# Kernel optimization log

Hardware: AMD Instinct MI355X
Metric: run time of the kernel (lower is better)

Reference implementation:

```python
import jax, jax.numpy as jnp
import numpy as np

MD = 4  # max displacement -> 9x9 = 81 window, matches the +8 pad and 81 output channels


def setup_inputs() -> dict:
    key = jax.random.key(0)
    k1, k2 = jax.random.split(key)
    first = jax.random.normal(k1, (8, 256, 96, 128), dtype=jnp.float32)
    second = jax.random.normal(k2, (8, 256, 96, 128), dtype=jnp.float32)
    return {"first": first, "second": second}


def reference(first, second):
    # first, second: [B, C, H, W]
    B, C, H, W = first.shape
    # pad second spatially by MD on each side (the rbot1 [B, H+8, W+8, C] buffer)
    pad = jnp.pad(second, ((0, 0), (0, 0), (MD, MD), (MD, MD)))
    outs = []
    # channel ordering matches CUDA kernel: top_channel = (dy+4)*9 + (dx+4)
    for dy in range(2 * MD + 1):
        for dx in range(2 * MD + 1):
            shifted = jax.lax.dynamic_slice(pad, (0, 0, dy, dx), (B, C, H, W))
            outs.append(jnp.einsum('bchw,bchw->bhw', first, shifted))
    # kernel divides the per-pixel dot product by the channel count
    return jnp.stack(outs, axis=1) / C  # [B, 81, H, W]
```

## Files before the change

### kernel.cpp

```cpp
#include <hip/hip_runtime.h>

namespace {
constexpr int Bn = 8, Cn = 256, Hn = 96, Wn = 128;
constexpr int HWn = Hn * Wn;
constexpr int CHWn = Cn * HWn;
constexpr int ND = 9;
constexpr int STRIDE = 140;
constexpr int TILESH = Hn / 4;
constexpr int NBLK = Bn * TILESH * ND;
constexpr int PERX = NBLK / 8;
}

__global__ __launch_bounds__(64) void corr_kernel(
    const float* __restrict__ first, const float* __restrict__ second,
    float* __restrict__ out)
{
  __shared__ __align__(16) float sbuf[2][4 * STRIDE];

  const int lane = threadIdx.x;
  const int bid = blockIdx.x;
  const int logical = (bid & 7) * PERX + (bid >> 3);
  const int dy = logical % ND;
  const int t = logical / ND;
  const int b = t / TILESH;
  const int h0 = (t % TILESH) * 4;

  const int hs = lane >> 4;
  const int w0 = (lane & 15) << 3;

  const int r0 = lane >> 5;
  const int cc = lane & 31;

  const int gr0 = h0 + dy - 4 + r0;
  const int gr1 = gr0 + 2;
  const float m0 = (gr0 >= 0 && gr0 < Hn) ? 1.0f : 0.0f;
  const float m1 = (gr1 >= 0 && gr1 < Hn) ? 1.0f : 0.0f;
  const int cg0 = min(max(gr0, 0), Hn - 1);
  const int cg1 = min(max(gr1, 0), Hn - 1);

  const float* src0 = second + b * CHWn + cg0 * Wn + 4 * cc;
  const float* src1 = second + b * CHWn + cg1 * Wn + 4 * cc;
  const float* fsrc = first + b * CHWn + (h0 + hs) * Wn + w0;

  const int dw0 = STRIDE * r0 + 4 + 4 * cc;
  const int dw1 = STRIDE * (r0 + 2) + 4 + 4 * cc;
  const int srw = STRIDE * hs + w0;

  if (lane < 16) {
    const int bsel = lane >> 3;
    const int row = (lane >> 1) & 3;
    const int side = lane & 1;
    *(float4*)&sbuf[bsel][STRIDE * row + (side ? 132 : 0)] =
        make_float4(0.f, 0.f, 0.f, 0.f);
  }

  float acc[ND][8];
#pragma unroll
  for (int dx = 0; dx < ND; ++dx)
#pragma unroll
    for (int p = 0; p < 8; ++p) acc[dx][p] = 0.f;

  float4 st0 = *(const float4*)src0;
  float4 st1 = *(const float4*)src1;
  float4 fa = *(const float4*)fsrc;
  float4 fb = *(const float4*)(fsrc + 4);
  src0 += HWn; src1 += HWn; fsrc += HWn;
  st0.x *= m0; st0.y *= m0; st0.z *= m0; st0.w *= m0;
  st1.x *= m1; st1.y *= m1; st1.z *= m1; st1.w *= m1;
  *(float4*)&sbuf[0][dw0] = st0;
  *(float4*)&sbuf[0][dw1] = st1;

#pragma unroll 2
  for (int c = 0; c < Cn; ++c) {
    const int cur = c & 1;
    float4 nst0, nst1, nfa, nfb;
    if (c < Cn - 1) {
      nst0 = *(const float4*)src0;
      nst1 = *(const float4*)src1;
      nfa = *(const float4*)fsrc;
      nfb = *(const float4*)(fsrc + 4);
      src0 += HWn; src1 += HWn; fsrc += HWn;
    } else {
      nst0 = nst1 = nfa = nfb = make_float4(0.f, 0.f, 0.f, 0.f);
    }

    const float* sb = &sbuf[cur][srw];
    float4 q0 = *(const float4*)(sb + 0);
    float4 q1 = *(const float4*)(sb + 4);
    float4 q2 = *(const float4*)(sb + 8);
    float4 q3 = *(const float4*)(sb + 12);
    const float s[16] = {q0.x, q0.y, q0.z, q0.w, q1.x, q1.y, q1.z, q1.w,
                         q2.x, q2.y, q2.z, q2.w, q3.x, q3.y, q3.z, q3.w};
    const float f[8] = {fa.x, fa.y, fa.z, fa.w, fb.x, fb.y, fb.z, fb.w};

#pragma unroll
    for (int dx = 0; dx < ND; ++dx)
#pragma unroll
      for (int p = 0; p < 8; ++p)
        acc[dx][p] = fmaf(f[p], s[p + dx], acc[dx][p]);

    if (c < Cn - 1) {
      nst0.x *= m0; nst0.y *= m0; nst0.z *= m0; nst0.w *= m0;
      nst1.x *= m1; nst1.y *= m1; nst1.z *= m1; nst1.w *= m1;
      const int nxt = cur ^ 1;
      *(float4*)&sbuf[nxt][dw0] = nst0;
      *(float4*)&sbuf[nxt][dw1] = nst1;
    }
    fa = nfa; fb = nfb;
  }

  const float sc = 1.0f / Cn;
  float* obase = out + ((b * 81 + dy * ND) * Hn + (h0 + hs)) * Wn + w0;
#pragma unroll
  for (int dx = 0; dx < ND; ++dx) {
    float4 o0 = make_float4(acc[dx][0] * sc, acc[dx][1] * sc,
                            acc[dx][2] * sc, acc[dx][3] * sc);
    float4 o1 = make_float4(acc[dx][4] * sc, acc[dx][5] * sc,
                            acc[dx][6] * sc, acc[dx][7] * sc);
    *(float4*)(obase + dx * HWn) = o0;
    *(float4*)(obase + dx * HWn + 4) = o1;
  }
}

extern "C" void kernel_launch(void* const* d_in, const int* in_sizes, int n_in,
                              void* d_out, int out_size, void* d_ws, size_t ws_size,
                              hipStream_t stream) {
  const float* first = (const float*)d_in[0];
  const float* second = (const float*)d_in[1];
  float* out = (float*)d_out;
  corr_kernel<<<dim3(NBLK), dim3(64), 0, stream>>>(first, second, out);
}
```

Before: 120.7 us.

## Replace LDS staging of shifted rows with DPP lane shifts and deeper prefetch

Each lane now loads its own 8 values of the padded second-image row and gets the 4 left and 4 right neighbours from adjacent lanes through DPP row_shr/row_shl moves. This removes the shared-memory double buffer along with its writes and reads, and out-of-range edge lanes are zero-filled by bound_ctrl. The channel loop now prefetches two channels ahead with explicit register staging, and launch bounds request 2 blocks per CU. In exchange there are more VALU moves per channel and higher register pressure from the larger prefetch.

```diff
diff --git a/kernel.cpp b/kernel.cpp
--- a/kernel.cpp
+++ b/kernel.cpp
@@ -5,18 +5,28 @@
 constexpr int HWn = Hn * Wn;
 constexpr int CHWn = Cn * HWn;
 constexpr int ND = 9;
-constexpr int STRIDE = 140;
 constexpr int TILESH = Hn / 4;
 constexpr int NBLK = Bn * TILESH * ND;
 constexpr int PERX = NBLK / 8;
 }
 
-__global__ __launch_bounds__(64) void corr_kernel(
+__device__ __forceinline__ float dpp_shr1(float x) {
+  return __int_as_float(__builtin_amdgcn_update_dpp(
+      0, __float_as_int(x), 0x111 , 0xF, 0xF, true));
+}
+__device__ __forceinline__ float dpp_shl1(float x) {
+  return __int_as_float(__builtin_amdgcn_update_dpp(
+      0, __float_as_int(x), 0x101 , 0xF, 0xF, true));
+}
+
+struct Ch {
+  float4 sa, sb, fa, fb;
+};
+
+__global__ __launch_bounds__(64, 2) void corr_kernel(
     const float* __restrict__ first, const float* __restrict__ second,
     float* __restrict__ out)
 {
-  __shared__ __align__(16) float sbuf[2][4 * STRIDE];
-
   const int lane = threadIdx.x;
   const int bid = blockIdx.x;
   const int logical = (bid & 7) * PERX + (bid >> 3);
@@ -28,31 +38,12 @@
   const int hs = lane >> 4;
   const int w0 = (lane & 15) << 3;
 
-  const int r0 = lane >> 5;
-  const int cc = lane & 31;
+  const int gr = h0 + hs + dy - 4;
+  const float m = (gr >= 0 && gr < Hn) ? 1.0f : 0.0f;
+  const int cg = min(max(gr, 0), Hn - 1);
 
-  const int gr0 = h0 + dy - 4 + r0;
-  const int gr1 = gr0 + 2;
-  const float m0 = (gr0 >= 0 && gr0 < Hn) ? 1.0f : 0.0f;
-  const float m1 = (gr1 >= 0 && gr1 < Hn) ? 1.0f : 0.0f;
-  const int cg0 = min(max(gr0, 0), Hn - 1);
-  const int cg1 = min(max(gr1, 0), Hn - 1);
-
-  const float* src0 = second + b * CHWn + cg0 * Wn + 4 * cc;
-  const float* src1 = second + b * CHWn + cg1 * Wn + 4 * cc;
+  const float* ssrc = second + b * CHWn + cg * Wn + w0;
   const float* fsrc = first + b * CHWn + (h0 + hs) * Wn + w0;
-
-  const int dw0 = STRIDE * r0 + 4 + 4 * cc;
-  const int dw1 = STRIDE * (r0 + 2) + 4 + 4 * cc;
-  const int srw = STRIDE * hs + w0;
-
-  if (lane < 16) {
-    const int bsel = lane >> 3;
-    const int row = (lane >> 1) & 3;
-    const int side = lane & 1;
-    *(float4*)&sbuf[bsel][STRIDE * row + (side ? 132 : 0)] =
-        make_float4(0.f, 0.f, 0.f, 0.f);
-  }
 
   float acc[ND][8];
 #pragma unroll
@@ -60,54 +51,47 @@
 #pragma unroll
     for (int p = 0; p < 8; ++p) acc[dx][p] = 0.f;
 
-  float4 st0 = *(const float4*)src0;
-  float4 st1 = *(const float4*)src1;
-  float4 fa = *(const float4*)fsrc;
-  float4 fb = *(const float4*)(fsrc + 4);
-  src0 += HWn; src1 += HWn; fsrc += HWn;
-  st0.x *= m0; st0.y *= m0; st0.z *= m0; st0.w *= m0;
-  st1.x *= m1; st1.y *= m1; st1.z *= m1; st1.w *= m1;
-  *(float4*)&sbuf[0][dw0] = st0;
-  *(float4*)&sbuf[0][dw1] = st1;
+  auto LOADCH = [&](int coff) -> Ch {
+    Ch r;
+    r.sa = *(const float4*)(ssrc + coff);
+    r.sb = *(const float4*)(ssrc + coff + 4);
+    r.fa = *(const float4*)(fsrc + coff);
+    r.fb = *(const float4*)(fsrc + coff + 4);
+    return r;
+  };
 
-#pragma unroll 2
-  for (int c = 0; c < Cn; ++c) {
-    const int cur = c & 1;
-    float4 nst0, nst1, nfa, nfb;
-    if (c < Cn - 1) {
-      nst0 = *(const float4*)src0;
-      nst1 = *(const float4*)src1;
-      nfa = *(const float4*)fsrc;
-      nfb = *(const float4*)(fsrc + 4);
-      src0 += HWn; src1 += HWn; fsrc += HWn;
-    } else {
-      nst0 = nst1 = nfa = nfb = make_float4(0.f, 0.f, 0.f, 0.f);
-    }
-
-    const float* sb = &sbuf[cur][srw];
-    float4 q0 = *(const float4*)(sb + 0);
-    float4 q1 = *(const float4*)(sb + 4);
-    float4 q2 = *(const float4*)(sb + 8);
-    float4 q3 = *(const float4*)(sb + 12);
-    const float s[16] = {q0.x, q0.y, q0.z, q0.w, q1.x, q1.y, q1.z, q1.w,
-                         q2.x, q2.y, q2.z, q2.w, q3.x, q3.y, q3.z, q3.w};
-    const float f[8] = {fa.x, fa.y, fa.z, fa.w, fb.x, fb.y, fb.z, fb.w};
-
+  auto COMP = [&](const Ch& ch) {
+    const float sa0 = ch.sa.x * m, sa1 = ch.sa.y * m, sa2 = ch.sa.z * m, sa3 = ch.sa.w * m;
+    const float sb0 = ch.sb.x * m, sb1 = ch.sb.y * m, sb2 = ch.sb.z * m, sb3 = ch.sb.w * m;
+    const float s[16] = {
+        dpp_shr1(sb0), dpp_shr1(sb1), dpp_shr1(sb2), dpp_shr1(sb3),
+        sa0, sa1, sa2, sa3,
+        sb0, sb1, sb2, sb3,
+        dpp_shl1(sa0), dpp_shl1(sa1), dpp_shl1(sa2), dpp_shl1(sa3)};
+    const float f[8] = {ch.fa.x, ch.fa.y, ch.fa.z, ch.fa.w,
+                        ch.fb.x, ch.fb.y, ch.fb.z, ch.fb.w};
 #pragma unroll
     for (int dx = 0; dx < ND; ++dx)
 #pragma unroll
       for (int p = 0; p < 8; ++p)
         acc[dx][p] = fmaf(f[p], s[p + dx], acc[dx][p]);
+  };
 
-    if (c < Cn - 1) {
-      nst0.x *= m0; nst0.y *= m0; nst0.z *= m0; nst0.w *= m0;
-      nst1.x *= m1; nst1.y *= m1; nst1.z *= m1; nst1.w *= m1;
-      const int nxt = cur ^ 1;
-      *(float4*)&sbuf[nxt][dw0] = nst0;
-      *(float4*)&sbuf[nxt][dw1] = nst1;
-    }
-    fa = nfa; fb = nfb;
+  Ch L0 = LOADCH(0);
+  Ch L1 = LOADCH(HWn);
+  int coff = 2 * HWn;
+#pragma unroll 1
+  for (int it = 0; it < (Cn - 2) / 2; ++it) {
+    Ch N0 = LOADCH(coff);
+    Ch N1 = LOADCH(coff + HWn);
+    COMP(L0);
+    COMP(L1);
+    L0 = N0;
+    L1 = N1;
+    coff += 2 * HWn;
   }
+  COMP(L0);
+  COMP(L1);
 
   const float sc = 1.0f / Cn;
   float* obase = out + ((b * 81 + dy * ND) * Hn + (h0 + hs)) * Wn + w0;
```

Result: faster. 98.27 us (-18.6%).
